# Kernel tuning notes

Hardware: AMD Instinct MI355X
Metric: run time of the kernel (lower is better)

Reference implementation:

```python
import jax, jax.numpy as jnp
import numpy as np


def setup_inputs() -> dict:
    key = jax.random.key(0)
    ks = jax.random.split(key, 12)
    B, L, D, M, T = 8, 512, 1024, 64, 8
    p = lambda k, shape: jax.random.normal(k, shape, jnp.float32) * 0.02
    return {
        "hid": jax.random.normal(ks[0], (B, L, D), jnp.float32),
        "sp_width": jax.random.randint(ks[1], (B, L), 0, T),
        "Wq_st": p(ks[2], (D, D)), "bq_st": jnp.zeros((D,), jnp.float32),
        "Wk_st": p(ks[3], (D, D)), "bk_st": jnp.zeros((D,), jnp.float32),
        "rel_st": p(ks[4], (2 * M + 1, D)),
        "Wq_ed": p(ks[5], (D, D)), "bq_ed": jnp.zeros((D,), jnp.float32),
        "Wk_ed": p(ks[6], (D, D)), "bk_ed": jnp.zeros((D,), jnp.float32),
        "rel_ed": p(ks[7], (2 * M + 1, D)),
        "comb_W": p(ks[8], (D, 2 * D)), "comb_b": jnp.zeros((D,), jnp.float32),
        "max_sp_len": T,
    }


def _rel_ids(L, M):
    # clipped relative position j - i, shifted to [0, 2M]
    d = jnp.arange(L)[None, :] - jnp.arange(L)[:, None]
    return jnp.clip(d, -M, M) + M  # [L, L]


def _attn(hid, Wq, bq, Wk, bk, rel_emb, mask, r):
    # OpenNMT-style relative-position attention, head_count=1; returns probs [B,L,L]
    D = hid.shape[-1]
    q = (hid @ Wq.T + bq) / jnp.sqrt(jnp.asarray(D, hid.dtype))
    k = hid @ Wk.T + bk
    scores = jnp.einsum('bid,bjd->bij', q, k)
    qrel = jnp.einsum('bid,rd->bir', q, rel_emb)           # [B, L, 2M+1]
    scores = scores + jnp.take_along_axis(
        qrel, jnp.broadcast_to(r[None], scores.shape), axis=2)
    scores = jnp.where(mask[:, None, :] > 0, scores, jnp.asarray(-1e18, scores.dtype))
    return jax.nn.softmax(scores, axis=-1)


def _upd(hid, attn_w, comb_W, comb_b):
    # (hid.unsqueeze(1) * attn_w.unsqueeze(-1)).sum(2) == attn_w @ hid
    hidc = jnp.einsum('bij,bjd->bid', attn_w, hid)
    return jax.nn.relu(jnp.concatenate([hid, hidc], axis=-1) @ comb_W.T + comb_b)


def reference(hid, sp_width, Wq_st, bq_st, Wk_st, bk_st, rel_st,
              Wq_ed, bq_ed, Wk_ed, bk_ed, rel_ed, comb_W, comb_b, max_sp_len):
    L = hid.shape[1]
    M = (rel_st.shape[0] - 1) // 2
    r = _rel_ids(L, M)

    def step(carry, i):
        hid1, hid2 = carry
        mask = jnp.logical_and(sp_width != 0, i <= sp_width).astype(hid1.dtype)
        st = _attn(hid1, Wq_st, bq_st, Wk_st, bk_st, rel_st, mask, r)
        hid1 = _upd(hid1, st, comb_W, comb_b)
        ed = _attn(hid2, Wq_ed, bq_ed, Wk_ed, bk_ed, rel_ed, mask, r)
        hid2 = _upd(hid2, ed, comb_W, comb_b)
        return (hid1, hid2), (st, ed, mask)

    _, (sts, eds, masks) = jax.lax.scan(step, (hid, hid), jnp.arange(max_sp_len))
    # torch.stack(list, -2) -> [B, L, T, L]; torch.stack(masks, -1) -> [B, L, T]
    return (jnp.moveaxis(sts, 0, 2), jnp.moveaxis(eds, 0, 2), jnp.moveaxis(masks, 0, 2))
```

## Files before the change

kernel.cpp:

```cpp
#include <hip/hip_runtime.h>
#include <hip/hip_bf16.h>

namespace {

constexpr int Bb = 8;
constexpr int Lr = 512;
constexpr int Dd = 1024;
constexpr int Mm = 64;
constexpr int Tt = 8;
constexpr int BL = Bb * Lr;

constexpr size_t H    = (size_t)BL * Dd;
constexpr size_t SC   = (size_t)Bb * Lr * Lr;
constexpr size_t PS   = SC;
constexpr size_t GSZ  = (size_t)BL * 1280;
constexpr size_t WASZ = (size_t)1280 * Dd;

constexpr int TILE = 128 * 64;

typedef __attribute__((ext_vector_type(8))) short bf16x8;
typedef __attribute__((ext_vector_type(4))) float f32x4;

__device__ __forceinline__ short f2bf(float x) {
    __hip_bfloat16 h = __float2bfloat16(x);
    return *reinterpret_cast<short*>(&h);
}
__device__ __forceinline__ float bf2f(short s) {
    unsigned int u = ((unsigned int)(unsigned short)s) << 16;
    return __uint_as_float(u);
}

__device__ __forceinline__ void gemm_core(
    const short* __restrict__ A, int lda,
    const short* __restrict__ Bm, int ldb, int K,
    short* As, short* Bs, f32x4 acc[4][4])
{
    const int tid  = threadIdx.x;
    const int lane = tid & 63;
    const int w    = tid >> 6;
    const int wm   = w >> 1, wn = w & 1;
    const int lr   = lane >> 3;
    const int lc   = (lane & 7) << 3;

    for (int k0 = 0; k0 < K; k0 += 64) {
        #pragma unroll
        for (int i = 0; i < 4; ++i) {
            const int r0 = (i * 4 + w) * 8;
            const short* gA = A + (size_t)(r0 + lr) * lda + k0 + lc;
            __builtin_amdgcn_global_load_lds(
                (const __attribute__((address_space(1))) void*)gA,
                (__attribute__((address_space(3))) void*)(As + r0 * 64), 16, 0, 0);
            const short* gB = Bm + (size_t)(r0 + lr) * ldb + k0 + lc;
            __builtin_amdgcn_global_load_lds(
                (const __attribute__((address_space(1))) void*)gB,
                (__attribute__((address_space(3))) void*)(Bs + r0 * 64), 16, 0, 0);
        }
        __syncthreads();
        #pragma unroll
        for (int ks = 0; ks < 2; ++ks) {
            bf16x8 af[4], bb[4];
            #pragma unroll
            for (int f = 0; f < 4; ++f) {
                af[f] = *(const bf16x8*)(As + (wm * 64 + f * 16 + (lane & 15)) * 64
                                            + ks * 32 + ((lane >> 4) << 3));
                bb[f] = *(const bf16x8*)(Bs + (wn * 64 + f * 16 + (lane & 15)) * 64
                                            + ks * 32 + ((lane >> 4) << 3));
            }
            #pragma unroll
            for (int fm = 0; fm < 4; ++fm)
                #pragma unroll
                for (int fn = 0; fn < 4; ++fn)
                    acc[fm][fn] = __builtin_amdgcn_mfma_f32_16x16x32_bf16(
                        af[fm], bb[fn], acc[fm][fn], 0, 0, 0);
        }
        __syncthreads();
    }
}

__global__ __launch_bounds__(256)
void gg_k(const short* __restrict__ h0, const short* __restrict__ h1,
          const short* __restrict__ waug, const short* __restrict__ wc,
          short* __restrict__ g, short* __restrict__ x, short* __restrict__ yT)
{
    __shared__ short As[TILE], Bs[TILE];
    f32x4 acc[4][4] = {};
    const int xcd = blockIdx.x & 7;
    const int l   = blockIdx.x >> 3;
    const int nt  = l >> 3;
    const int mt  = xcd * 8 + (l & 7);
    const int s   = mt >> 5;
    const int m0  = (mt & 31) * 128;
    const short* h = s ? h1 : h0;
    const short* Bm; int ldb;
    if (nt < 10)      { Bm = waug + (size_t)s * WASZ + (size_t)nt * 128 * Dd; ldb = Dd; }
    else if (nt < 18) { Bm = wc + (size_t)(nt - 10) * 128 * 2048;             ldb = 2048; }
    else              { Bm = wc + 1024 + (size_t)(nt - 18) * 128 * 2048;      ldb = 2048; }
    gemm_core(h + (size_t)m0 * Dd, Dd, Bm, ldb, Dd, As, Bs, acc);

    const int lane = threadIdx.x & 63, w = threadIdx.x >> 6;
    const int wm = w >> 1, wn = w & 1;
    if (nt < 10) {
        short* out = g + (size_t)s * GSZ;
        #pragma unroll
        for (int fm = 0; fm < 4; ++fm)
            #pragma unroll
            for (int fn = 0; fn < 4; ++fn) {
                const int col = nt * 128 + wn * 64 + fn * 16 + (lane & 15);
                #pragma unroll
                for (int rr = 0; rr < 4; ++rr) {
                    const int ml = wm * 64 + fm * 16 + ((lane >> 4) << 2) + rr;
                    out[(size_t)(m0 + ml) * 1280 + col] = f2bf(acc[fm][fn][rr]);
                }
            }
    } else if (nt < 18) {
        short* out = x + (size_t)s * H;
        #pragma unroll
        for (int fm = 0; fm < 4; ++fm)
            #pragma unroll
            for (int fn = 0; fn < 4; ++fn) {
                const int col = (nt - 10) * 128 + wn * 64 + fn * 16 + (lane & 15);
                #pragma unroll
                for (int rr = 0; rr < 4; ++rr) {
                    const int ml = wm * 64 + fm * 16 + ((lane >> 4) << 2) + rr;
                    out[(size_t)(m0 + ml) * Dd + col] = f2bf(acc[fm][fn][rr]);
                }
            }
    } else {
        short* out = yT + (size_t)s * H;
        const int b = m0 >> 9;
        const int il_base = (m0 & 511) + wm * 64 + ((lane >> 4) << 2);
        #pragma unroll
        for (int fm = 0; fm < 4; ++fm)
            #pragma unroll
            for (int fn = 0; fn < 4; ++fn) {
                const int n = (nt - 18) * 128 + wn * 64 + fn * 16 + (lane & 15);
                short4 pk;
                short* pks = reinterpret_cast<short*>(&pk);
                #pragma unroll
                for (int rr = 0; rr < 4; ++rr) pks[rr] = f2bf(acc[fm][fn][rr]);
                *reinterpret_cast<short4*>(
                    &out[((size_t)b * Dd + n) * Lr + il_base + fm * 16]) = pk;
            }
    }
}

__global__ __launch_bounds__(256)
void scores2_k(const short* __restrict__ g,
               const short* __restrict__ h0, const short* __restrict__ h1,
               const float* __restrict__ rbv, float* __restrict__ scb)
{
    __shared__ short As[TILE], Bs[TILE];
    f32x4 acc[4][4] = {};
    const int sid = (blockIdx.x & 7) * 32 + (blockIdx.x >> 3);
    const int n0 = (sid & 3) * 128, m0 = ((sid >> 2) & 3) * 128;
    const int z = sid >> 4;
    const int s = z >> 3, b = z & 7;
    const short* gs = g + (size_t)s * GSZ;
    const short* A  = gs + (size_t)(b * Lr + m0) * 1280;
    const short* hB = (s ? h1 : h0) + (size_t)(b * Lr + n0) * Dd;
    gemm_core(A, 1280, hB, Dd, Dd, As, Bs, acc);

    float* out = scb + (size_t)s * SC;
    const float c = rbv[s * 132 + 129];
    const int lane = threadIdx.x & 63, w = threadIdx.x >> 6;
    const int wm = w >> 1, wn = w & 1;
    #pragma unroll
    for (int fm = 0; fm < 4; ++fm)
        #pragma unroll
        for (int fn = 0; fn < 4; ++fn) {
            const int j = n0 + wn * 64 + fn * 16 + (lane & 15);
            const float vj = bf2f(gs[(size_t)(b * Lr + j) * 1280 + 1154]);
            #pragma unroll
            for (int rr = 0; rr < 4; ++rr) {
                const int i = m0 + wm * 64 + fm * 16 + ((lane >> 4) << 2) + rr;
                const size_t grow = (size_t)(b * Lr + i) * 1280;
                const float ui = bf2f(gs[grow + 1153]);
                int d = j - i;
                d = d < -Mm ? -Mm : (d > Mm ? Mm : d);
                const int r = d + Mm;
                const float grel = bf2f(gs[grow + 1024 + r]);
                out[((size_t)b * Lr + i) * Lr + j] =
                    0.03125f * (acc[fm][fn][rr] + ui + vj + c + grel +
                                rbv[s * 132 + r]);
            }
        }
}

__global__ __launch_bounds__(256)
void softmax2_k(const float* __restrict__ scb, const int* __restrict__ spw,
                float* __restrict__ out0, float* __restrict__ out1,
                short* __restrict__ probs, int t)
{
    const int i = blockIdx.x, b = blockIdx.y, s = blockIdx.z;
    const float* srow = scb + (size_t)s * SC + ((size_t)b * Lr + i) * Lr;
    const int tidx = threadIdx.x;
    float s0, s1;
    {
        int w = spw[b * Lr + tidx];
        s0 = (w != 0 && t <= w) ? srow[tidx] : -1e18f;
        w = spw[b * Lr + tidx + 256];
        s1 = (w != 0 && t <= w) ? srow[tidx + 256] : -1e18f;
    }
    float mx = fmaxf(s0, s1);
    #pragma unroll
    for (int off = 32; off > 0; off >>= 1) mx = fmaxf(mx, __shfl_down(mx, off));
    __shared__ float redm[4], reds[4];
    const int lane = tidx & 63, wid = tidx >> 6;
    if (lane == 0) redm[wid] = mx;
    __syncthreads();
    mx = fmaxf(fmaxf(redm[0], redm[1]), fmaxf(redm[2], redm[3]));
    const float e0 = expf(s0 - mx), e1 = expf(s1 - mx);
    float sum = e0 + e1;
    #pragma unroll
    for (int off = 32; off > 0; off >>= 1) sum += __shfl_down(sum, off);
    if (lane == 0) reds[wid] = sum;
    __syncthreads();
    const float inv = 1.f / (reds[0] + reds[1] + reds[2] + reds[3]);
    const float p0 = e0 * inv, p1 = e1 * inv;
    float* orow = (s ? out1 : out0) + (((size_t)b * Lr + i) * Tt + t) * Lr;
    orow[tidx]       = p0;
    orow[tidx + 256] = p1;
    short* prow = probs + (size_t)s * PS + ((size_t)b * Lr + i) * Lr;
    prow[tidx]       = f2bf(p0);
    prow[tidx + 256] = f2bf(p1);
}

__global__ __launch_bounds__(256)
void pv2_k(const short* __restrict__ probs, const short* __restrict__ yT,
           const short* __restrict__ x, const float* __restrict__ cb,
           short* __restrict__ hn0, short* __restrict__ hn1)
{
    __shared__ short As[TILE], Bs[TILE];
    f32x4 acc[4][4] = {};
    const int sid = (blockIdx.x & 7) * 64 + (blockIdx.x >> 3);
    const int n0 = (sid & 7) * 128, m0 = ((sid >> 3) & 3) * 128;
    const int z = sid >> 5;
    const int s = z >> 3, b = z & 7;
    const short* A = probs + (size_t)s * PS + (size_t)(b * Lr + m0) * Lr;
    const short* B = yT + (size_t)s * H + (size_t)(b * Dd + n0) * Lr;
    gemm_core(A, Lr, B, Lr, Lr, As, Bs, acc);

    short* hout = s ? hn1 : hn0;
    const short* xs = x + (size_t)s * H;
    const int lane = threadIdx.x & 63, w = threadIdx.x >> 6;
    const int wm = w >> 1, wn = w & 1;
    #pragma unroll
    for (int fm = 0; fm < 4; ++fm)
        #pragma unroll
        for (int fn = 0; fn < 4; ++fn) {
            const int n = n0 + wn * 64 + fn * 16 + (lane & 15);
            const float bias = cb[n];
            #pragma unroll
            for (int rr = 0; rr < 4; ++rr) {
                const int row = b * Lr + m0 + wm * 64 + fm * 16 +
                                ((lane >> 4) << 2) + rr;
                const float v = fmaxf(acc[fm][fn][rr] +
                                      bf2f(xs[(size_t)row * Dd + n]) + bias, 0.f);
                hout[(size_t)row * Dd + n] = f2bf(v);
            }
        }
}

__global__ __launch_bounds__(256)
void w2_k(const short* __restrict__ wqT0, const short* __restrict__ wqT1,
          const short* __restrict__ wkT0, const short* __restrict__ wkT1,
          short* __restrict__ waug)
{
    __shared__ short As[TILE], Bs[TILE];
    f32x4 acc[4][4] = {};
    const int s = blockIdx.x >> 6, rem = blockIdx.x & 63;
    const int m0 = (rem >> 3) * 128, n0 = (rem & 7) * 128;
    const short* A = (s ? wkT1 : wkT0) + (size_t)m0 * Dd;
    const short* B = (s ? wqT1 : wqT0) + (size_t)n0 * Dd;
    gemm_core(A, Dd, B, Dd, Dd, As, Bs, acc);
    short* out = waug + (size_t)s * WASZ;
    const int lane = threadIdx.x & 63, w = threadIdx.x >> 6;
    const int wm = w >> 1, wn = w & 1;
    #pragma unroll
    for (int fm = 0; fm < 4; ++fm)
        #pragma unroll
        for (int fn = 0; fn < 4; ++fn) {
            const int nl = n0 + wn * 64 + fn * 16 + (lane & 15);
            #pragma unroll
            for (int rr = 0; rr < 4; ++rr) {
                const int ml = m0 + wm * 64 + fm * 16 + ((lane >> 4) << 2) + rr;
                out[(size_t)ml * Dd + nl] = f2bf(acc[fm][fn][rr]);
            }
        }
}

__global__ __launch_bounds__(256)
void rw2_k(const short* __restrict__ relp0, const short* __restrict__ relp1,
           const short* __restrict__ wqT0, const short* __restrict__ wqT1,
           short* __restrict__ waug)
{
    __shared__ short As[TILE], Bs[TILE];
    f32x4 acc[4][4] = {};
    const int s = blockIdx.x >> 4, rem = blockIdx.x & 15;
    const int m0 = (rem >> 3) * 128, n0 = (rem & 7) * 128;
    const short* A = (s ? relp1 : relp0) + (size_t)m0 * Dd;
    const short* B = (s ? wqT1 : wqT0) + (size_t)n0 * Dd;
    gemm_core(A, Dd, B, Dd, Dd, As, Bs, acc);
    short* out = waug + (size_t)s * WASZ + (size_t)1024 * Dd;
    const int lane = threadIdx.x & 63, w = threadIdx.x >> 6;
    const int wm = w >> 1, wn = w & 1;
    #pragma unroll
    for (int fm = 0; fm < 4; ++fm)
        #pragma unroll
        for (int fn = 0; fn < 4; ++fn) {
            const int nl = n0 + wn * 64 + fn * 16 + (lane & 15);
            #pragma unroll
            for (int rr = 0; rr < 4; ++rr) {
                const int ml = m0 + wm * 64 + fm * 16 + ((lane >> 4) << 2) + rr;
                out[(size_t)ml * Dd + nl] = f2bf(acc[fm][fn][rr]);
            }
        }
}

__global__ __launch_bounds__(64)
void uv_k(const short* __restrict__ wqT0, const short* __restrict__ wqT1,
          const short* __restrict__ wkT0, const short* __restrict__ wkT1,
          const float* __restrict__ bq0, const float* __restrict__ bq1,
          const float* __restrict__ bk0, const float* __restrict__ bk1,
          short* __restrict__ waug)
{
    const int e = blockIdx.x, kind = blockIdx.y, s = blockIdx.z;
    const short* wT  = kind ? (s ? wkT1 : wkT0) : (s ? wqT1 : wqT0);
    const float* vec = kind ? (s ? bq1 : bq0) : (s ? bk1 : bk0);
    float sum = 0.f;
    for (int d = threadIdx.x; d < Dd; d += 64)
        sum += bf2f(wT[(size_t)e * Dd + d]) * vec[d];
    #pragma unroll
    for (int off = 32; off > 0; off >>= 1) sum += __shfl_down(sum, off);
    if (threadIdx.x == 0)
        waug[(size_t)s * WASZ + (size_t)(1153 + kind) * Dd + e] = f2bf(sum);
}

__global__ __launch_bounds__(64)
void rb_k(const float* __restrict__ rel0, const float* __restrict__ rel1,
          const float* __restrict__ bq0, const float* __restrict__ bq1,
          const float* __restrict__ bk0, const float* __restrict__ bk1,
          float* __restrict__ rbv)
{
    const int r = blockIdx.x, s = blockIdx.y;
    const float* bq = s ? bq1 : bq0;
    float sum = 0.f;
    if (r < 129) {
        const float* rel = s ? rel1 : rel0;
        for (int n = threadIdx.x; n < Dd; n += 64)
            sum += rel[(size_t)r * Dd + n] * bq[n];
    } else {
        const float* bk = s ? bk1 : bk0;
        for (int n = threadIdx.x; n < Dd; n += 64)
            sum += bq[n] * bk[n];
    }
    #pragma unroll
    for (int off = 32; off > 0; off >>= 1) sum += __shfl_down(sum, off);
    if (threadIdx.x == 0) rbv[s * 132 + r] = sum;
}

__global__ __launch_bounds__(256)
void transpose_f2bf_k(const float* __restrict__ src, short* __restrict__ dst)
{
    __shared__ float tile[64][65];
    const int r0 = blockIdx.y * 64, c0 = blockIdx.x * 64;
    const int col = threadIdx.x & 63, row4 = threadIdx.x >> 6;
    #pragma unroll
    for (int rr = 0; rr < 16; ++rr)
        tile[row4 + rr * 4][col] = src[(size_t)(r0 + row4 + rr * 4) * Dd + c0 + col];
    __syncthreads();
    #pragma unroll
    for (int rr = 0; rr < 16; ++rr)
        dst[(size_t)(c0 + row4 + rr * 4) * Dd + r0 + col] =
            f2bf(tile[col][row4 + rr * 4]);
}

__global__ void masks_k(const int* __restrict__ spw, float* __restrict__ out2)
{
    const int idx = blockIdx.x * 256 + threadIdx.x;
    if (idx < BL) {
        const int w = spw[idx];
        #pragma unroll
        for (int t = 0; t < Tt; ++t)
            out2[(size_t)idx * Tt + t] = (w != 0 && t <= w) ? 1.f : 0.f;
    }
}

__global__ void f2bf_k(const float* __restrict__ src, short* __restrict__ dst, int n)
{
    const int idx = blockIdx.x * 256 + threadIdx.x;
    if (idx < n) dst[idx] = f2bf(src[idx]);
}

__global__ void relpad_k(const float* __restrict__ rel, short* __restrict__ dst)
{
    const int idx = blockIdx.x * 256 + threadIdx.x;
    if (idx < 256 * 1024) {
        const int row = idx >> 10;
        dst[idx] = (row < 129) ? f2bf(rel[idx]) : (short)0;
    }
}

__global__ void hidinit_k(const float* __restrict__ hid,
                          short* __restrict__ h_st, short* __restrict__ h_ed)
{
    const int idx = blockIdx.x * 256 + threadIdx.x;
    if (idx < BL * Dd) {
        const short s = f2bf(hid[idx]);
        h_st[idx] = s;
        h_ed[idx] = s;
    }
}

}

extern "C" void kernel_launch(void* const* d_in, const int* in_sizes, int n_in,
                              void* d_out, int out_size, void* d_ws, size_t ws_size,
                              hipStream_t stream)
{
    const float* hid  = (const float*)d_in[0];
    const int*   spw  = (const int*)d_in[1];
    const float* Wq[2] = {(const float*)d_in[2], (const float*)d_in[7]};
    const float* bq[2] = {(const float*)d_in[3], (const float*)d_in[8]};
    const float* Wk[2] = {(const float*)d_in[4], (const float*)d_in[9]};
    const float* bk[2] = {(const float*)d_in[5], (const float*)d_in[10]};
    const float* rel[2]= {(const float*)d_in[6], (const float*)d_in[11]};
    const float* combW = (const float*)d_in[12];
    const float* combB = (const float*)d_in[13];

    float* out0 = (float*)d_out;
    float* out1 = out0 + (size_t)BL * Tt * Lr;
    float* out2 = out1 + (size_t)BL * Tt * Lr;

    short* wsS = (short*)d_ws;
    size_t cur = 0;
    short* hbuf[2][2];
    hbuf[0][0] = wsS + cur; cur += H;
    hbuf[0][1] = wsS + cur; cur += H;
    hbuf[1][0] = wsS + cur; cur += H;
    hbuf[1][1] = wsS + cur; cur += H;
    short* g   = wsS + cur; cur += 2 * GSZ;
    short* x   = wsS + cur; cur += 2 * H;
    short* yT  = wsS + cur; cur += 2 * H;
    short* probs = wsS + cur; cur += 2 * PS;
    short* waug  = wsS + cur; cur += 2 * WASZ;
    short* combWb = wsS + cur; cur += (size_t)Dd * 2 * Dd;
    short* relp[2];
    relp[0] = wsS + cur; cur += (size_t)256 * Dd;
    relp[1] = wsS + cur; cur += (size_t)256 * Dd;
    float* wsF = (float*)(wsS + cur);
    float* rbv = wsF;
    float* scb = wsF + 2 * 132;
    short* wqT[2] = {(short*)scb, (short*)scb + (size_t)Dd * Dd};
    short* wkT[2] = {(short*)scb + 2 * (size_t)Dd * Dd,
                     (short*)scb + 3 * (size_t)Dd * Dd};

    const int DD = Dd * Dd;
    f2bf_k<<<dim3((2 * DD + 255) / 256), 256, 0, stream>>>(combW, combWb, 2 * DD);
    relpad_k<<<dim3(256 * Dd / 256), 256, 0, stream>>>(rel[0], relp[0]);
    relpad_k<<<dim3(256 * Dd / 256), 256, 0, stream>>>(rel[1], relp[1]);
    transpose_f2bf_k<<<dim3(16, 16), 256, 0, stream>>>(Wq[0], wqT[0]);
    transpose_f2bf_k<<<dim3(16, 16), 256, 0, stream>>>(Wq[1], wqT[1]);
    transpose_f2bf_k<<<dim3(16, 16), 256, 0, stream>>>(Wk[0], wkT[0]);
    transpose_f2bf_k<<<dim3(16, 16), 256, 0, stream>>>(Wk[1], wkT[1]);
    w2_k<<<dim3(128), 256, 0, stream>>>(wqT[0], wqT[1], wkT[0], wkT[1], waug);
    rw2_k<<<dim3(32), 256, 0, stream>>>(relp[0], relp[1], wqT[0], wqT[1], waug);
    uv_k<<<dim3(1024, 2, 2), 64, 0, stream>>>(wqT[0], wqT[1], wkT[0], wkT[1],
                                              bq[0], bq[1], bk[0], bk[1], waug);
    rb_k<<<dim3(130, 2), 64, 0, stream>>>(rel[0], rel[1], bq[0], bq[1],
                                          bk[0], bk[1], rbv);
    hidinit_k<<<dim3((int)(H / 256)), 256, 0, stream>>>(hid, hbuf[0][0], hbuf[1][0]);
    masks_k<<<dim3((BL + 255) / 256), 256, 0, stream>>>(spw, out2);

    int curb = 0;
    for (int t = 0; t < Tt; ++t) {
        short* h0 = hbuf[0][curb], *h1 = hbuf[1][curb];
        short* hn0 = hbuf[0][curb ^ 1], *hn1 = hbuf[1][curb ^ 1];
        gg_k<<<dim3(1664), 256, 0, stream>>>(h0, h1, waug, combWb, g, x, yT);
        scores2_k<<<dim3(256), 256, 0, stream>>>(g, h0, h1, rbv, scb);
        softmax2_k<<<dim3(Lr, Bb, 2), 256, 0, stream>>>(scb, spw, out0, out1, probs, t);
        pv2_k<<<dim3(512), 256, 0, stream>>>(probs, yT, x, combB, hn0, hn1);
        curb ^= 1;
    }
}
```

Measured before the change: 1.505 ms.

## Rewrite gg_k GEMM as 256x256 tile with async LDS double-buffered pipeline

Replaces the 128x128 gg_k GEMM, which used a shared gemm_core, with a 256x256 tile on 512 threads. Global tiles go straight into LDS through global_load_lds into a double buffer with XOR swizzling. Each k-step is split into four phases, each with fine-grained vmcnt waits and barriers, so the next tile's loads overlap the MFMA work, and s_setprio raises priority during the MFMA bursts. The larger tile reuses more data per load, but it needs more registers (an 8x4 accumulator array) and cuts the grid from 1664 to 416 blocks, which may leave CUs underused.

```diff
diff --git a/kernel.cpp b/kernel.cpp
--- a/kernel.cpp
+++ b/kernel.cpp
@@ -77,69 +77,162 @@
     }
 }
 
-__global__ __launch_bounds__(256)
+template<int Q>
+__device__ __forceinline__ void gg_phase_mfma(
+    const short* __restrict__ Ab, f32x4 (&acc)[8][4], const bf16x8 (&bq)[4][2],
+    int wm, int lane, int hi3, int sw)
+{
+    bf16x8 a[2][2];
+    #pragma unroll
+    for (int e = 0; e < 2; ++e)
+        #pragma unroll
+        for (int ks = 0; ks < 2; ++ks)
+            a[e][ks] = *(const bf16x8*)(Ab + (Q * 64 + wm * 32 + e * 16 + (lane & 15)) * 64
+                                           + ((ks * 32 + hi3) ^ sw));
+    __builtin_amdgcn_s_setprio(1);
+    #pragma unroll
+    for (int fn = 0; fn < 4; ++fn)
+        #pragma unroll
+        for (int e = 0; e < 2; ++e)
+            #pragma unroll
+            for (int ks = 0; ks < 2; ++ks)
+                acc[2 * Q + e][fn] = __builtin_amdgcn_mfma_f32_16x16x32_bf16(
+                    a[e][ks], bq[fn][ks], acc[2 * Q + e][fn], 0, 0, 0);
+    __builtin_amdgcn_s_setprio(0);
+}
+
+__global__ __launch_bounds__(512, 2)
 void gg_k(const short* __restrict__ h0, const short* __restrict__ h1,
           const short* __restrict__ waug, const short* __restrict__ wc,
           short* __restrict__ g, short* __restrict__ x, short* __restrict__ yT)
 {
-    __shared__ short As[TILE], Bs[TILE];
-    f32x4 acc[4][4] = {};
+    __shared__ short lds[65536];
+    f32x4 acc[8][4] = {};
+    bf16x8 bq[4][2];
+    const int tid  = threadIdx.x;
+    const int lane = tid & 63;
+    const int w    = tid >> 6;
+    const int wm   = w >> 2, wn = w & 3;
+
     const int xcd = blockIdx.x & 7;
     const int l   = blockIdx.x >> 3;
-    const int nt  = l >> 3;
-    const int mt  = xcd * 8 + (l & 7);
-    const int s   = mt >> 5;
-    const int m0  = (mt & 31) * 128;
+    const int nt  = l >> 2;
+    const int mt  = xcd * 4 + (l & 3);
+    const int s   = mt >> 4;
+    const int m0  = (mt & 15) * 256;
     const short* h = s ? h1 : h0;
-    const short* Bm; int ldb;
-    if (nt < 10)      { Bm = waug + (size_t)s * WASZ + (size_t)nt * 128 * Dd; ldb = Dd; }
-    else if (nt < 18) { Bm = wc + (size_t)(nt - 10) * 128 * 2048;             ldb = 2048; }
-    else              { Bm = wc + 1024 + (size_t)(nt - 18) * 128 * 2048;      ldb = 2048; }
-    gemm_core(h + (size_t)m0 * Dd, Dd, Bm, ldb, Dd, As, Bs, acc);
-
-    const int lane = threadIdx.x & 63, w = threadIdx.x >> 6;
-    const int wm = w >> 1, wn = w & 1;
-    if (nt < 10) {
+    const short* Bg; int ldb;
+    if (nt < 5)      { Bg = waug + (size_t)s * WASZ + (size_t)nt * 256 * Dd; ldb = Dd; }
+    else if (nt < 9) { Bg = wc + (size_t)(nt - 5) * 256 * 2048;              ldb = 2048; }
+    else             { Bg = wc + 1024 + (size_t)(nt - 9) * 256 * 2048;       ldb = 2048; }
+    const short* Ag = h + (size_t)m0 * Dd;
+
+    const int lr      = tid >> 3;
+    const int gcol    = ((tid & 7) * 8) ^ ((lr & 7) << 3);
+    const int arowoff = lr + (lr < 32 ? 0 : 96);
+
+    auto stA = [&](int kt, int pb, int q) {
+        const short* src = Ag + (size_t)(q * 32 + arowoff) * Dd + kt * 64 + gcol;
+        short* dst = lds + pb * 32768 + q * 4096 + tid * 8;
+        __builtin_amdgcn_global_load_lds(
+            (const __attribute__((address_space(1))) void*)src,
+            (__attribute__((address_space(3))) void*)dst, 16, 0, 0);
+    };
+    auto stB = [&](int kt, int pb, int u) {
+        const short* src = Bg + (size_t)(u * 64 + lr) * ldb + kt * 64 + gcol;
+        short* dst = lds + pb * 32768 + 16384 + u * 4096 + tid * 8;
+        __builtin_amdgcn_global_load_lds(
+            (const __attribute__((address_space(1))) void*)src,
+            (__attribute__((address_space(3))) void*)dst, 16, 0, 0);
+    };
+
+    stB(0, 0, 0); stB(0, 0, 1); stB(0, 0, 2); stB(0, 0, 3);
+    stA(0, 0, 0); stA(0, 0, 1); stA(0, 0, 2); stA(0, 0, 3);
+
+    const int hi3 = (lane >> 4) << 3;
+    const int sw  = (lane & 7) << 3;
+
+    int p = 0;
+    for (int kt = 0; kt < 16; ++kt, p ^= 1) {
+        const short* Ab = lds + p * 32768;
+        const short* Bb = lds + p * 32768 + 16384;
+        const int ktn = kt + 1;
+        const bool nl = (ktn < 16);
+        asm volatile("s_waitcnt vmcnt(3)" ::: "memory");
+        __builtin_amdgcn_s_barrier();
+        __builtin_amdgcn_sched_barrier(0);
+        if (nl) { stB(ktn, p ^ 1, 0); stB(ktn, p ^ 1, 1); }
+        #pragma unroll
+        for (int fn = 0; fn < 4; ++fn) {
+            bq[fn][0] = *(const bf16x8*)(Bb + (wn * 64 + fn * 16 + (lane & 15)) * 64
+                                            + ((0 + hi3) ^ sw));
+            bq[fn][1] = *(const bf16x8*)(Bb + (wn * 64 + fn * 16 + (lane & 15)) * 64
+                                            + ((32 + hi3) ^ sw));
+        }
+        gg_phase_mfma<0>(Ab, acc, bq, wm, lane, hi3, sw);
+        if (nl) asm volatile("s_waitcnt vmcnt(4)" ::: "memory");
+        else    asm volatile("s_waitcnt vmcnt(2)" ::: "memory");
+        __builtin_amdgcn_s_barrier();
+        __builtin_amdgcn_sched_barrier(0);
+        if (nl) { stB(ktn, p ^ 1, 2); stB(ktn, p ^ 1, 3); }
+        gg_phase_mfma<1>(Ab, acc, bq, wm, lane, hi3, sw);
+        if (nl) asm volatile("s_waitcnt vmcnt(5)" ::: "memory");
+        else    asm volatile("s_waitcnt vmcnt(1)" ::: "memory");
+        __builtin_amdgcn_s_barrier();
+        __builtin_amdgcn_sched_barrier(0);
+        if (nl) { stA(ktn, p ^ 1, 0); stA(ktn, p ^ 1, 1); }
+        gg_phase_mfma<2>(Ab, acc, bq, wm, lane, hi3, sw);
+        if (nl) asm volatile("s_waitcnt vmcnt(6)" ::: "memory");
+        else    asm volatile("s_waitcnt vmcnt(0)" ::: "memory");
+        __builtin_amdgcn_s_barrier();
+        __builtin_amdgcn_sched_barrier(0);
+        if (nl) { stA(ktn, p ^ 1, 2); stA(ktn, p ^ 1, 3); }
+        gg_phase_mfma<3>(Ab, acc, bq, wm, lane, hi3, sw);
+    }
+
+    const int r4 = (lane >> 4) << 2;
+    const int cb = wn * 64 + (lane & 15);
+    if (nt < 5) {
         short* out = g + (size_t)s * GSZ;
         #pragma unroll
-        for (int fm = 0; fm < 4; ++fm)
+        for (int fm = 0; fm < 8; ++fm)
             #pragma unroll
             for (int fn = 0; fn < 4; ++fn) {
-                const int col = nt * 128 + wn * 64 + fn * 16 + (lane & 15);
+                const int col = nt * 256 + cb + fn * 16;
                 #pragma unroll
                 for (int rr = 0; rr < 4; ++rr) {
-                    const int ml = wm * 64 + fm * 16 + ((lane >> 4) << 2) + rr;
-                    out[(size_t)(m0 + ml) * 1280 + col] = f2bf(acc[fm][fn][rr]);
+                    const int row = m0 + wm * 128 + fm * 16 + r4 + rr;
+                    out[(size_t)row * 1280 + col] = f2bf(acc[fm][fn][rr]);
                 }
             }
-    } else if (nt < 18) {
+    } else if (nt < 9) {
         short* out = x + (size_t)s * H;
         #pragma unroll
-        for (int fm = 0; fm < 4; ++fm)
+        for (int fm = 0; fm < 8; ++fm)
             #pragma unroll
             for (int fn = 0; fn < 4; ++fn) {
-                const int col = (nt - 10) * 128 + wn * 64 + fn * 16 + (lane & 15);
+                const int col = (nt - 5) * 256 + cb + fn * 16;
                 #pragma unroll
                 for (int rr = 0; rr < 4; ++rr) {
-                    const int ml = wm * 64 + fm * 16 + ((lane >> 4) << 2) + rr;
-                    out[(size_t)(m0 + ml) * Dd + col] = f2bf(acc[fm][fn][rr]);
+                    const int row = m0 + wm * 128 + fm * 16 + r4 + rr;
+                    out[(size_t)row * Dd + col] = f2bf(acc[fm][fn][rr]);
                 }
             }
     } else {
         short* out = yT + (size_t)s * H;
         const int b = m0 >> 9;
-        const int il_base = (m0 & 511) + wm * 64 + ((lane >> 4) << 2);
-        #pragma unroll
-        for (int fm = 0; fm < 4; ++fm)
+        const int il0 = (m0 & 511) + wm * 128 + r4;
+        #pragma unroll
+        for (int fm = 0; fm < 8; ++fm)
             #pragma unroll
             for (int fn = 0; fn < 4; ++fn) {
-                const int n = (nt - 18) * 128 + wn * 64 + fn * 16 + (lane & 15);
+                const int n = (nt - 9) * 256 + cb + fn * 16;
                 short4 pk;
                 short* pks = reinterpret_cast<short*>(&pk);
                 #pragma unroll
                 for (int rr = 0; rr < 4; ++rr) pks[rr] = f2bf(acc[fm][fn][rr]);
                 *reinterpret_cast<short4*>(
-                    &out[((size_t)b * Dd + n) * Lr + il_base + fm * 16]) = pk;
+                    &out[((size_t)b * Dd + n) * Lr + il0 + fm * 16]) = pk;
             }
     }
 }
@@ -476,7 +569,7 @@
     for (int t = 0; t < Tt; ++t) {
         short* h0 = hbuf[0][curb], *h1 = hbuf[1][curb];
         short* hn0 = hbuf[0][curb ^ 1], *hn1 = hbuf[1][curb ^ 1];
-        gg_k<<<dim3(1664), 256, 0, stream>>>(h0, h1, waug, combWb, g, x, yT);
+        gg_k<<<dim3(416), 512, 0, stream>>>(h0, h1, waug, combWb, g, x, yT);
         scores2_k<<<dim3(256), 256, 0, stream>>>(g, h0, h1, rbv, scb);
         softmax2_k<<<dim3(Lr, Bb, 2), 256, 0, stream>>>(scb, spw, out0, out1, probs, t);
         pv2_k<<<dim3(512), 256, 0, stream>>>(probs, yT, x, combB, hn0, hn1);
```

Measured after the change: 1.226 ms. -18.6%, faster.
